# Performance work log

Measured on AMD Instinct MI355X. Metric: run time of the kernel, lower is better.

## Reference

```python
import jax, jax.numpy as jnp
import numpy as np

B, FEAT = 2048, 256
NUM_PIDS, CQ_SIZE = 30000, 8192
MOMENTUM = 0.5
SCALAR = 30.0
EPS_BN = 1e-5      # BatchNorm1d default eps
EPS_NORM = 1e-12   # F.normalize default eps


def l2norm(x):
    n = jnp.linalg.norm(x, axis=1, keepdims=True)
    return x / jnp.maximum(n, EPS_NORM)


def setup_inputs() -> dict:
    key = jax.random.key(0)
    k1, k2, k3, k4 = jax.random.split(key, 4)
    inputs = jax.random.normal(k1, (B, FEAT), jnp.float32)
    label = jax.random.randint(k2, (B,), 0, NUM_PIDS + 1)  # NUM_PIDS == ignore_index
    lut = jax.random.normal(k3, (NUM_PIDS, FEAT), jnp.float32)
    cq = jax.random.normal(k4, (CQ_SIZE, FEAT), jnp.float32)
    bn_weight = jnp.ones((FEAT,), jnp.float32)
    bn_bias = jnp.zeros((FEAT,), jnp.float32)
    return {"inputs": inputs, "label": label, "lut": lut, "cq": cq,
            "bn_weight": bn_weight, "bn_bias": bn_bias}


def reference(inputs, label, lut, cq, bn_weight, bn_bias):
    dtype = inputs.dtype
    rows = jnp.arange(B)

    # --- eval-mode BN on inputs (running stats at init: mean=0, var=1) ---
    norm_inputs = inputs / jnp.sqrt(jnp.asarray(1.0 + EPS_BN, dtype)) * bn_weight + bn_bias

    # --- bad-row masks (rows that are all zero) ---
    bad_lut_mask = jnp.all(lut == 0, axis=1)            # [P]
    good_lut = ~bad_lut_mask
    lc = jnp.minimum(label, NUM_PIDS - 1)
    bad_pos_mask = (label < NUM_PIDS) & bad_lut_mask[lc]  # label hits a bad lut row

    # --- train-mode masked BN over good lut rows (momentum=1.0 => running stats = batch stats) ---
    gm = good_lut[:, None].astype(dtype)
    n = jnp.sum(gm)
    mean = jnp.sum(lut * gm, axis=0) / n
    var = jnp.sum(((lut - mean) ** 2) * gm, axis=0) / n  # biased var for normalization
    lut_bn = jnp.where(good_lut[:, None],
                       (lut - mean) / jnp.sqrt(var + EPS_BN) * bn_weight + bn_bias,
                       lut)
    # running stats update happens under the hood (detached); unbiased var
    rm1 = jax.lax.stop_gradient(mean)
    rv1 = jax.lax.stop_gradient(var * n / (n - 1.0))

    qn = l2norm(norm_inputs)                              # [B, F]
    out_lab = qn @ l2norm(lut_bn).T                       # [B, P]
    out_lab = jnp.where(bad_lut_mask[None, :], jnp.asarray(-1.0, dtype), out_lab)
    out_lab = out_lab.at[rows, lc].set(
        jnp.where(bad_pos_mask, jnp.asarray(1.0, dtype), out_lab[rows, lc]))

    # --- eval-mode masked BN on cq using the just-updated running stats ---
    bad_cq_mask = jnp.all(cq == 0, axis=1)                # [Q]
    cq_bn = jnp.where(~bad_cq_mask[:, None],
                      (cq - rm1) / jnp.sqrt(rv1 + EPS_BN) * bn_weight + bn_bias,
                      cq)
    out_unl = qn @ l2norm(cq_bn).T                        # [B, Q]
    out_unl = jnp.where(bad_cq_mask[None, :], jnp.asarray(-1.0, dtype), out_unl)

    projected = jnp.concatenate([out_lab, out_unl], axis=1) * jnp.asarray(SCALAR, dtype)

    # --- cross entropy with ignore_index = NUM_PIDS, reduction='none', then sum/B ---
    logp = jax.nn.log_softmax(projected, axis=1)
    valid = label != NUM_PIDS
    per = -logp[rows, jnp.where(valid, label, 0)]
    per = jnp.where(valid, per, jnp.asarray(0.0, dtype))
    loss = jnp.sum(per) / B

    # --- serial momentum scatter into lut + circular-buffer enqueue into cq ---
    xs = jax.lax.stop_gradient(inputs)
    lut0 = jax.lax.stop_gradient(lut)
    cq0 = jax.lax.stop_gradient(cq)

    def step(carry, xy):
        lut_c, cq_c, hdr = carry
        x, y = xy
        is_lab = y < NUM_PIDS
        yc = jnp.minimum(y, NUM_PIDS - 1)
        new_row = jnp.where(is_lab, MOMENTUM * lut_c[yc] + (1.0 - MOMENTUM) * x, lut_c[yc])
        lut_c = lut_c.at[yc].set(new_row)
        cq_row = jnp.where(is_lab, cq_c[hdr], x)
        cq_c = cq_c.at[hdr].set(cq_row)
        hdr = jnp.where(is_lab, hdr, (hdr + 1) % CQ_SIZE)
        return (lut_c, cq_c, hdr), None

    (new_lut, new_cq, _), _ = jax.lax.scan(
        step, (lut0, cq0, jnp.asarray(0, label.dtype)), (xs, label))

    return loss, new_lut, new_cq
```

## Files before the change

kernel.cpp:

```cpp
#include <hip/hip_runtime.h>
#include <math.h>

#define NUM_PIDS 30000
#define CQ_SIZE  8192
#define BATCH    2048
#define FEAT     256
#define EPS_BN   1e-5f
#define EPS_NORM 1e-12f
#define SCALARV  30.0f

#define LUT_PAD  30080
#define NCOL     38272
#define BC       128
#define LUT_TILES 235
#define CT       299
#define RT       16
#define NWG      (CT*RT)
#define NB1      240
#define ROWS1    125
#define QPLANE   (BATCH*FEAT)

#define WS_Q1    0
#define WS_CB1   (WS_Q1 + BATCH*FEAT)
#define WS_CB2   (WS_CB1 + BATCH)
#define WS_RN2   (WS_CB2 + BATCH)
#define WS_FLAGS (WS_RN2 + 2*NCOL)
#define WS_PSUM  (WS_FLAGS + LUT_PAD)
#define WS_PSQ   (WS_PSUM + NB1*FEAT)
#define WS_PCNT  (WS_PSQ + NB1*FEAT)
#define WS_A1    (WS_PCNT + 256)
#define WS_B1    (WS_A1 + FEAT)
#define WS_A2    (WS_B1 + FEAT)
#define WS_B2    (WS_A2 + FEAT)
#define WS_ZT    (WS_B2 + FEAT)
#define WS_PART  (WS_ZT + BATCH)
#define WS_LOSS8 (WS_PART + BATCH*CT)
#define WS_XH    ((WS_LOSS8 + 8 + 3) & ~3)
#define WS_XL    (WS_XH + NCOL*FEAT/2)
#define WS_QP    (WS_XL + NCOL*FEAT/2)

typedef __bf16 bf16x8 __attribute__((ext_vector_type(8)));
typedef float  f32x4  __attribute__((ext_vector_type(4)));

__device__ __forceinline__ unsigned short f2bf(float f) {
  __bf16 h = (__bf16)f; return __builtin_bit_cast(unsigned short, h);
}
__device__ __forceinline__ float bf2f(unsigned short u) {
  __bf16 h = __builtin_bit_cast(__bf16, u); return (float)h;
}
__device__ __forceinline__ void gload_lds16(const void* g, void* l) {
  __builtin_amdgcn_global_load_lds((__attribute__((address_space(1))) void*)(g),
                                   (__attribute__((address_space(3))) void*)(l), 16, 0, 0);
}

__global__ __launch_bounds__(256) void k_stats1(const float* __restrict__ lut,
                                                float* __restrict__ ws,
                                                int* __restrict__ flags) {
  const int t = threadIdx.x;
  const int rbase = blockIdx.x * ROWS1;
  __shared__ unsigned char wz[ROWS1 * 4];
  float s = 0.f, sq = 0.f;
  for (int i = 0; i < ROWS1; ++i) {
    float v = lut[(size_t)(rbase + i) * FEAT + t];
    s += v; sq += v * v;
    unsigned long long bal = __ballot(v != 0.0f);
    if ((t & 63) == 0) wz[i * 4 + (t >> 6)] = (bal != 0ull) ? 1 : 0;
  }
  __syncthreads();
  for (int i = t; i < ROWS1; i += 256) {
    int bad = !(wz[i*4] | wz[i*4+1] | wz[i*4+2] | wz[i*4+3]);
    flags[rbase + i] = bad;
  }
  ws[WS_PSUM + blockIdx.x * FEAT + t] = s;
  ws[WS_PSQ  + blockIdx.x * FEAT + t] = sq;
  if (t == 0) {
    int cnt = 0;
    for (int i = 0; i < ROWS1; ++i)
      cnt += (wz[i*4] | wz[i*4+1] | wz[i*4+2] | wz[i*4+3]) ? 1 : 0;
    ws[WS_PCNT + blockIdx.x] = (float)cnt;
  }
}

__global__ __launch_bounds__(256) void k_stats2(const float* __restrict__ bnw,
                                                const float* __restrict__ bnb,
                                                float* __restrict__ ws) {
  const int t = threadIdx.x;
  float2* rn2 = (float2*)(ws + WS_RN2);
  float s = 0.f, sq = 0.f, n = 0.f;
  for (int b = 0; b < NB1; ++b) { s += ws[WS_PSUM + b*FEAT + t]; sq += ws[WS_PSQ + b*FEAT + t]; }
  for (int b = 0; b < NB1; ++b) n += ws[WS_PCNT + b];
  float mean = s / n;
  float var = fmaxf(sq / n - mean * mean, 0.f);
  float istd_b = rsqrtf(var + EPS_BN);
  float rv1 = var * n / (n - 1.f);
  float istd_u = rsqrtf(rv1 + EPS_BN);
  float w = bnw[t], b_ = bnb[t];
  float a1 = istd_b * w, a2 = istd_u * w;
  ws[WS_A1 + t] = a1; ws[WS_B1 + t] = b_ - mean * a1;
  ws[WS_A2 + t] = a2; ws[WS_B2 + t] = b_ - mean * a2;
  if (t < (LUT_PAD - NUM_PIDS)) rn2[NUM_PIDS + t] = make_float2(0.f, -1e30f);
}

__global__ __launch_bounds__(256) void k_prep(const float* __restrict__ lut,
                                              const float* __restrict__ cq,
                                              float* __restrict__ ws,
                                              unsigned short* __restrict__ xh,
                                              unsigned short* __restrict__ xl) {
  const int row = blockIdx.x * 4 + (threadIdx.x >> 6);
  const int ln = threadIdx.x & 63;
  float2* rn2 = (float2*)(ws + WS_RN2);
  if (row >= NUM_PIDS && row < LUT_PAD) {
    uint2 z = make_uint2(0u, 0u);
    *(uint2*)(xh + (size_t)row * FEAT + ln * 4) = z;
    *(uint2*)(xl + (size_t)row * FEAT + ln * 4) = z;
    return;
  }
  const float* src; const float* av; const float* bv;
  if (row < NUM_PIDS) {
    src = lut + (size_t)row * FEAT; av = ws + WS_A1; bv = ws + WS_B1;
  } else {
    src = cq + (size_t)(row - LUT_PAD) * FEAT; av = ws + WS_A2; bv = ws + WS_B2;
  }
  float4 x = ((const float4*)src)[ln];
  float4 a = ((const float4*)av)[ln];
  float4 b = ((const float4*)bv)[ln];
  unsigned short h0 = f2bf(x.x), h1 = f2bf(x.y), h2 = f2bf(x.z), h3 = f2bf(x.w);
  unsigned short l0 = f2bf(x.x - bf2f(h0)), l1 = f2bf(x.y - bf2f(h1));
  unsigned short l2 = f2bf(x.z - bf2f(h2)), l3 = f2bf(x.w - bf2f(h3));
  *(uint2*)(xh + (size_t)row * FEAT + ln * 4) =
      make_uint2((unsigned)h0 | ((unsigned)h1 << 16), (unsigned)h2 | ((unsigned)h3 << 16));
  *(uint2*)(xl + (size_t)row * FEAT + ln * 4) =
      make_uint2((unsigned)l0 | ((unsigned)l1 << 16), (unsigned)l2 | ((unsigned)l3 << 16));
  bool nz = (x.x != 0.f) || (x.y != 0.f) || (x.z != 0.f) || (x.w != 0.f);
  unsigned long long bal = __ballot(nz);
  float t0 = a.x*x.x + b.x, t1 = a.y*x.y + b.y, t2 = a.z*x.z + b.z, t3 = a.w*x.w + b.w;
  float ssum = t0*t0 + t1*t1 + t2*t2 + t3*t3;
  for (int o = 32; o; o >>= 1) ssum += __shfl_xor(ssum, o);
  if (ln == 0) {
    rn2[row] = (bal == 0ull) ? make_float2(0.f, -SCALARV)
                             : make_float2(1.0f / fmaxf(sqrtf(ssum), EPS_NORM), 1e30f);
  }
}

__global__ __launch_bounds__(256) void k_qn(const float* __restrict__ inp,
                                            const float* __restrict__ bnw,
                                            const float* __restrict__ bnb,
                                            float* __restrict__ ws,
                                            unsigned short* __restrict__ qp) {
  const int r = blockIdx.x, t = threadIdx.x;
  const float s0 = rsqrtf(1.0f + EPS_BN);
  float v = inp[(size_t)r * FEAT + t];
  float bn = v * (bnw[t] * s0) + bnb[t];
  float x = bn * bn;
  for (int o = 32; o; o >>= 1) x += __shfl_down(x, o);
  __shared__ float w4[4];
  __shared__ float w8[8];
  if ((t & 63) == 0) w4[t >> 6] = x;
  __syncthreads();
  float nsq = w4[0] + w4[1] + w4[2] + w4[3];
  float rinv = 1.0f / fmaxf(sqrtf(nsq), EPS_NORM);
  float qn = bn * rinv;
  float y1 = qn * ws[WS_B1 + t], y2 = qn * ws[WS_B2 + t];
  for (int o = 32; o; o >>= 1) { y1 += __shfl_down(y1, o); y2 += __shfl_down(y2, o); }
  if ((t & 63) == 0) { w8[t >> 6] = y1; w8[4 + (t >> 6)] = y2; }
  float q1 = qn * ws[WS_A1 + t], q2 = qn * ws[WS_A2 + t];
  ws[WS_Q1 + (size_t)r * FEAT + t] = q1;
  size_t o1 = (size_t)r * FEAT + t;
  unsigned short h1 = f2bf(q1), h2 = f2bf(q2);
  qp[0*QPLANE + o1] = h1;
  qp[1*QPLANE + o1] = f2bf(q1 - bf2f(h1));
  qp[2*QPLANE + o1] = h2;
  qp[3*QPLANE + o1] = f2bf(q2 - bf2f(h2));
  __syncthreads();
  if (t == 0) {
    ws[WS_CB1 + r] = w8[0] + w8[1] + w8[2] + w8[3];
    ws[WS_CB2 + r] = w8[4] + w8[5] + w8[6] + w8[7];
  }
}

__global__ __launch_bounds__(256, 3) void k_gemm(const unsigned short* __restrict__ xh,
                                                 const unsigned short* __restrict__ xl,
                                                 const unsigned short* __restrict__ qp,
                                                 float* __restrict__ ws) {
  __shared__ __align__(16) unsigned char smem[32768];
  const int tid = threadIdx.x;
  const int w = tid >> 6, l = tid & 63;
  const int bid = blockIdx.x;
  const int sid = (bid & 7) * (NWG / 8) + (bid >> 3);
  const int colT = sid >> 4, rowT = sid & 15;
  const bool islut = colT < LUT_TILES;
  const int colbase = colT * BC;
  const int rowbase = rowT * 128;

  const unsigned short* qh = qp + (islut ? 0 : 2) * QPLANE;
  const unsigned short* ql = qh + QPLANE;

  const unsigned short* sg = (w & 1) ? xl : xh;
  unsigned char* sl = smem + (w & 1) * 16384 + (w >> 1) * 8192;
  const int segc = l >> 3;
  const int kc8l = (l & 7) ^ segc;
  const unsigned short* gp =
      sg + (size_t)(colbase + (w >> 1) * 64 + segc) * FEAT + kc8l * 8;

  const int lc = l & 15, lk = l >> 4;
  const int wr = w >> 1, wc = w & 1;
  const size_t qbase = (size_t)(rowbase + wr * 64 + lc) * FEAT;

  f32x4 acc[4][4];
#pragma unroll
  for (int rf = 0; rf < 4; ++rf)
#pragma unroll
    for (int cf = 0; cf < 4; ++cf) { f32x4 z = {0.f,0.f,0.f,0.f}; acc[rf][cf] = z; }

  for (int kc = 0; kc < 4; ++kc) {
    const int kb = kc * 64;
#pragma unroll
    for (int i = 0; i < 8; ++i)
      gload_lds16(gp + (size_t)i * 8 * FEAT + kb, sl + i * 1024);
    __syncthreads();
#pragma unroll
    for (int ks = 0; ks < 2; ++ks) {
      const int kc8 = ks * 4 + lk;
      const int sA = (kc8 ^ (lc & 7)) * 16;
      bf16x8 ah[4], al[4], bh[4], bl[4];
#pragma unroll
      for (int rf = 0; rf < 4; ++rf) {
        size_t qa = qbase + rf * 16 * FEAT + kb + kc8 * 8;
        ah[rf] = *(const bf16x8*)(qh + qa);
        al[rf] = *(const bf16x8*)(ql + qa);
      }
#pragma unroll
      for (int cf = 0; cf < 4; ++cf) {
        int off = (wc * 64 + cf * 16 + lc) * 128 + sA;
        bh[cf] = *(const bf16x8*)(smem + off);
        bl[cf] = *(const bf16x8*)(smem + 16384 + off);
      }
#pragma unroll
      for (int rf = 0; rf < 4; ++rf)
#pragma unroll
        for (int cf = 0; cf < 4; ++cf) {
          acc[rf][cf] = __builtin_amdgcn_mfma_f32_16x16x32_bf16(ah[rf], bh[cf], acc[rf][cf], 0, 0, 0);
          acc[rf][cf] = __builtin_amdgcn_mfma_f32_16x16x32_bf16(ah[rf], bl[cf], acc[rf][cf], 0, 0, 0);
          acc[rf][cf] = __builtin_amdgcn_mfma_f32_16x16x32_bf16(al[rf], bh[cf], acc[rf][cf], 0, 0, 0);
        }
    }
    __syncthreads();
  }

  const float* cb = ws + (islut ? WS_CB1 : WS_CB2);
  const float2* rn2 = (const float2*)(ws + WS_RN2);
  float* red = (float*)smem;
#pragma unroll
  for (int rf = 0; rf < 4; ++rf) {
    float cbv[4];
#pragma unroll
    for (int r4 = 0; r4 < 4; ++r4)
      cbv[r4] = cb[rowbase + wr * 64 + rf * 16 + lk * 4 + r4];
    float part[4] = {0.f, 0.f, 0.f, 0.f};
#pragma unroll
    for (int cf = 0; cf < 4; ++cf) {
      float2 rc = rn2[colbase + wc * 64 + cf * 16 + lc];
#pragma unroll
      for (int r4 = 0; r4 < 4; ++r4) {
        float z = SCALARV * rc.x * (acc[rf][cf][r4] + cbv[r4]);
        z = fminf(z, rc.y);
        part[r4] += __expf(z - SCALARV);
      }
    }
#pragma unroll
    for (int r4 = 0; r4 < 4; ++r4) {
#pragma unroll
      for (int o = 1; o < 16; o <<= 1) part[r4] += __shfl_xor(part[r4], o);
      if (lc == 0) red[(wr * 64 + rf * 16 + lk * 4 + r4) * 2 + wc] = part[r4];
    }
  }
  __syncthreads();
  if (tid < 128) {
    float val = red[tid * 2] + red[tid * 2 + 1];
    ws[WS_PART + (size_t)colT * BATCH + rowbase + tid] = val;
  }
}

__global__ __launch_bounds__(256) void k_target(const int* __restrict__ label,
                                                const float* __restrict__ lut,
                                                float* __restrict__ ws) {
  const int r = blockIdx.x, t = threadIdx.x;
  const int* flags = (const int*)(ws + WS_FLAGS);
  const float2* rn2 = (const float2*)(ws + WS_RN2);
  int y = label[r];
  if (y >= NUM_PIDS) { if (t == 0) ws[WS_ZT + r] = 0.f; return; }
  if (flags[y] == 1) { if (t == 0) ws[WS_ZT + r] = SCALARV; return; }
  float x = ws[WS_Q1 + (size_t)r * FEAT + t] * lut[(size_t)y * FEAT + t];
  for (int o = 32; o; o >>= 1) x += __shfl_down(x, o);
  __shared__ float w4[4];
  if ((t & 63) == 0) w4[t >> 6] = x;
  __syncthreads();
  if (t == 0) {
    float dot = w4[0] + w4[1] + w4[2] + w4[3];
    ws[WS_ZT + r] = SCALARV * rn2[y].x * (dot + ws[WS_CB1 + r]);
  }
}

__global__ __launch_bounds__(256) void k_loss(const int* __restrict__ label,
                                              float* __restrict__ ws) {
  const int t = threadIdx.x;
  const int r = blockIdx.x * 256 + t;
  const int* flags = (const int*)(ws + WS_FLAGS);
  float ls = 0.f;
  int y = label[r];
  if (y < NUM_PIDS) {
    float ss = 0.f;
    const float* p = ws + WS_PART;
    for (int c = 0; c < CT; ++c) ss += p[(size_t)c * BATCH + r];
    if (flags[y] == 1) ss += 1.0f - __expf(-2.0f * SCALARV);
    ls = (SCALARV + __logf(ss)) - ws[WS_ZT + r];
  }
  for (int o = 32; o; o >>= 1) ls += __shfl_down(ls, o);
  __shared__ float w4[4];
  if ((t & 63) == 0) w4[t >> 6] = ls;
  __syncthreads();
  if (t == 0) ws[WS_LOSS8 + blockIdx.x] = w4[0] + w4[1] + w4[2] + w4[3];
}

__global__ void k_loss2(float* __restrict__ ws, float* __restrict__ out) {
  if (threadIdx.x == 0) {
    float s = 0.f;
    for (int i = 0; i < 8; ++i) s += ws[WS_LOSS8 + i];
    out[0] = s / (float)BATCH;
  }
}

__global__ __launch_bounds__(256) void k_lutupd(const int* __restrict__ label,
                                                const float* __restrict__ inp,
                                                const float* __restrict__ lut,
                                                float* __restrict__ out_lut) {
  const int r = blockIdx.x, t = threadIdx.x;
  const int y = label[r];
  if (y >= NUM_PIDS) return;
  __shared__ unsigned long long mask[32];
  const int wv = t >> 6, ln = t & 63;
#pragma unroll
  for (int it = 0; it < 8; ++it) {
    int i = it * 256 + wv * 64 + ln;
    unsigned long long bal = __ballot(label[i] == y);
    if (ln == 0) mask[it * 4 + wv] = bal;
  }
  __syncthreads();
  const int wr_ = r >> 6, br_ = r & 63;
  unsigned long long selfbit = 1ull << br_;
  bool after = (mask[wr_] & ~((selfbit - 1) | selfbit)) != 0ull;
  for (int w2 = wr_ + 1; w2 < 32; ++w2) after = after || (mask[w2] != 0ull);
  if (after) return;
  float f = lut[(size_t)y * FEAT + t];
  for (int w2 = 0; w2 <= wr_; ++w2) {
    unsigned long long m = mask[w2];
    if (w2 == wr_) m &= (selfbit - 1) | selfbit;
    while (m) {
      int b = __ffsll((unsigned long long)m) - 1;
      m &= m - 1;
      int rr = w2 * 64 + b;
      f = 0.5f * f + 0.5f * inp[(size_t)rr * FEAT + t];
    }
  }
  out_lut[(size_t)y * FEAT + t] = f;
}

__global__ __launch_bounds__(256) void k_cqupd(const int* __restrict__ label,
                                               const float* __restrict__ inp,
                                               float* __restrict__ out_cq) {
  const int r = blockIdx.x, t = threadIdx.x;
  if (label[r] != NUM_PIDS) return;
  __shared__ unsigned long long mask[32];
  const int wv = t >> 6, ln = t & 63;
#pragma unroll
  for (int it = 0; it < 8; ++it) {
    int i = it * 256 + wv * 64 + ln;
    unsigned long long bal = __ballot(label[i] == NUM_PIDS);
    if (ln == 0) mask[it * 4 + wv] = bal;
  }
  __syncthreads();
  const int wr_ = r >> 6, br_ = r & 63;
  int rank = 0;
  for (int w2 = 0; w2 < wr_; ++w2) rank += __popcll(mask[w2]);
  rank += __popcll(mask[wr_] & ((1ull << br_) - 1ull));
  out_cq[(size_t)rank * FEAT + t] = inp[(size_t)r * FEAT + t];
}

extern "C" void kernel_launch(void* const* d_in, const int* in_sizes, int n_in,
                              void* d_out, int out_size, void* d_ws, size_t ws_size,
                              hipStream_t stream) {
  const float* inp = (const float*)d_in[0];
  const int* label = (const int*)d_in[1];
  const float* lut = (const float*)d_in[2];
  const float* cq  = (const float*)d_in[3];
  const float* bnw = (const float*)d_in[4];
  const float* bnb = (const float*)d_in[5];
  float* out = (float*)d_out;
  float* ws  = (float*)d_ws;
  int* flags = (int*)(ws + WS_FLAGS);
  unsigned short* xh = (unsigned short*)(ws + WS_XH);
  unsigned short* xl = (unsigned short*)(ws + WS_XL);
  unsigned short* qp = (unsigned short*)(ws + WS_QP);

  float* out_lut = out + 1;
  float* out_cq  = out + 1 + (size_t)NUM_PIDS * FEAT;

  hipMemcpyAsync(out_lut, lut, (size_t)NUM_PIDS * FEAT * sizeof(float),
                 hipMemcpyDeviceToDevice, stream);
  hipMemcpyAsync(out_cq, cq, (size_t)CQ_SIZE * FEAT * sizeof(float),
                 hipMemcpyDeviceToDevice, stream);

  k_stats1<<<NB1, 256, 0, stream>>>(lut, ws, flags);
  k_stats2<<<1, 256, 0, stream>>>(bnw, bnb, ws);
  k_prep<<<NCOL / 4, 256, 0, stream>>>(lut, cq, ws, xh, xl);
  k_qn<<<BATCH, 256, 0, stream>>>(inp, bnw, bnb, ws, qp);
  k_gemm<<<NWG, 256, 0, stream>>>(xh, xl, qp, ws);
  k_target<<<BATCH, 256, 0, stream>>>(label, lut, ws);
  k_loss<<<8, 256, 0, stream>>>(label, ws);
  k_loss2<<<1, 64, 0, stream>>>(ws, out);
  k_lutupd<<<BATCH, 256, 0, stream>>>(label, inp, lut, out_lut);
  k_cqupd<<<BATCH, 256, 0, stream>>>(label, inp, out_cq);
}
```

Baseline: 383.3 us.

## Fuse output copies into prep, target into qn, stage Q tiles in LDS

The separate device-to-device copies of lut and cq into the outputs are removed and done inside k_prep, which already reads every row. The target-logit dot product moves into k_qn, which drops the fp32 Q workspace write, and the lut and cq update kernels are merged into one launched before the GEMM. The GEMM now stages both Q planes into a 64KB LDS buffer instead of reading them from global memory per fragment, and drops its occupancy hint of 3. The changes cut launches and redundant memory traffic, at the cost of larger LDS use that may lower GEMM occupancy.

Measured after the change: 347.4 us. 9.4% less time.

```diff
diff --git a/kernel.cpp b/kernel.cpp
--- a/kernel.cpp
+++ b/kernel.cpp
@@ -105,7 +105,9 @@
                                               const float* __restrict__ cq,
                                               float* __restrict__ ws,
                                               unsigned short* __restrict__ xh,
-                                              unsigned short* __restrict__ xl) {
+                                              unsigned short* __restrict__ xl,
+                                              float* __restrict__ out_lut,
+                                              float* __restrict__ out_cq) {
   const int row = blockIdx.x * 4 + (threadIdx.x >> 6);
   const int ln = threadIdx.x & 63;
   float2* rn2 = (float2*)(ws + WS_RN2);
@@ -115,15 +117,18 @@
     *(uint2*)(xl + (size_t)row * FEAT + ln * 4) = z;
     return;
   }
-  const float* src; const float* av; const float* bv;
+  const float* src; const float* av; const float* bv; float* dst;
   if (row < NUM_PIDS) {
     src = lut + (size_t)row * FEAT; av = ws + WS_A1; bv = ws + WS_B1;
+    dst = out_lut + (size_t)row * FEAT;
   } else {
     src = cq + (size_t)(row - LUT_PAD) * FEAT; av = ws + WS_A2; bv = ws + WS_B2;
+    dst = out_cq + (size_t)(row - LUT_PAD) * FEAT;
   }
   float4 x = ((const float4*)src)[ln];
   float4 a = ((const float4*)av)[ln];
   float4 b = ((const float4*)bv)[ln];
+  dst[ln*4+0] = x.x; dst[ln*4+1] = x.y; dst[ln*4+2] = x.z; dst[ln*4+3] = x.w;
   unsigned short h0 = f2bf(x.x), h1 = f2bf(x.y), h2 = f2bf(x.z), h3 = f2bf(x.w);
   unsigned short l0 = f2bf(x.x - bf2f(h0)), l1 = f2bf(x.y - bf2f(h1));
   unsigned short l2 = f2bf(x.z - bf2f(h2)), l3 = f2bf(x.w - bf2f(h3));
@@ -145,6 +150,8 @@
 __global__ __launch_bounds__(256) void k_qn(const float* __restrict__ inp,
                                             const float* __restrict__ bnw,
                                             const float* __restrict__ bnb,
+                                            const int* __restrict__ label,
+                                            const float* __restrict__ lut,
                                             float* __restrict__ ws,
                                             unsigned short* __restrict__ qp) {
   const int r = blockIdx.x, t = threadIdx.x;
@@ -155,6 +162,7 @@
   for (int o = 32; o; o >>= 1) x += __shfl_down(x, o);
   __shared__ float w4[4];
   __shared__ float w8[8];
+  __shared__ float w4b[4];
   if ((t & 63) == 0) w4[t >> 6] = x;
   __syncthreads();
   float nsq = w4[0] + w4[1] + w4[2] + w4[3];
@@ -164,7 +172,6 @@
   for (int o = 32; o; o >>= 1) { y1 += __shfl_down(y1, o); y2 += __shfl_down(y2, o); }
   if ((t & 63) == 0) { w8[t >> 6] = y1; w8[4 + (t >> 6)] = y2; }
   float q1 = qn * ws[WS_A1 + t], q2 = qn * ws[WS_A2 + t];
-  ws[WS_Q1 + (size_t)r * FEAT + t] = q1;
   size_t o1 = (size_t)r * FEAT + t;
   unsigned short h1 = f2bf(q1), h2 = f2bf(q2);
   qp[0*QPLANE + o1] = h1;
@@ -176,13 +183,27 @@
     ws[WS_CB1 + r] = w8[0] + w8[1] + w8[2] + w8[3];
     ws[WS_CB2 + r] = w8[4] + w8[5] + w8[6] + w8[7];
   }
-}
-
-__global__ __launch_bounds__(256, 3) void k_gemm(const unsigned short* __restrict__ xh,
-                                                 const unsigned short* __restrict__ xl,
-                                                 const unsigned short* __restrict__ qp,
-                                                 float* __restrict__ ws) {
-  __shared__ __align__(16) unsigned char smem[32768];
+  const int* flags = (const int*)(ws + WS_FLAGS);
+  const float2* rn2 = (const float2*)(ws + WS_RN2);
+  int y = label[r];
+  if (y >= NUM_PIDS) { if (t == 0) ws[WS_ZT + r] = 0.f; return; }
+  if (flags[y] == 1) { if (t == 0) ws[WS_ZT + r] = SCALARV; return; }
+  float xt = q1 * lut[(size_t)y * FEAT + t];
+  for (int o = 32; o; o >>= 1) xt += __shfl_down(xt, o);
+  if ((t & 63) == 0) w4b[t >> 6] = xt;
+  __syncthreads();
+  if (t == 0) {
+    float dot = w4b[0] + w4b[1] + w4b[2] + w4b[3];
+    float cb1 = w8[0] + w8[1] + w8[2] + w8[3];
+    ws[WS_ZT + r] = SCALARV * rn2[y].x * (dot + cb1);
+  }
+}
+
+__global__ __launch_bounds__(256) void k_gemm(const unsigned short* __restrict__ xh,
+                                              const unsigned short* __restrict__ xl,
+                                              const unsigned short* __restrict__ qp,
+                                              float* __restrict__ ws) {
+  __shared__ __align__(16) unsigned char smem[65536];
   const int tid = threadIdx.x;
   const int w = tid >> 6, l = tid & 63;
   const int bid = blockIdx.x;
@@ -195,16 +216,18 @@
   const unsigned short* qh = qp + (islut ? 0 : 2) * QPLANE;
   const unsigned short* ql = qh + QPLANE;
 
-  const unsigned short* sg = (w & 1) ? xl : xh;
-  unsigned char* sl = smem + (w & 1) * 16384 + (w >> 1) * 8192;
-  const int segc = l >> 3;
-  const int kc8l = (l & 7) ^ segc;
-  const unsigned short* gp =
-      sg + (size_t)(colbase + (w >> 1) * 64 + segc) * FEAT + kc8l * 8;
+  const int segc = l >> 3, slot = l & 7;
+  const int kc8l = slot ^ segc;
+  const unsigned short* gsrc;
+  unsigned char* lbase;
+  int gbase;
+  if (w == 0)      { gsrc = xh; lbase = smem;         gbase = colbase; }
+  else if (w == 1) { gsrc = xl; lbase = smem + 16384; gbase = colbase; }
+  else if (w == 2) { gsrc = qh; lbase = smem + 32768; gbase = rowbase; }
+  else             { gsrc = ql; lbase = smem + 49152; gbase = rowbase; }
 
   const int lc = l & 15, lk = l >> 4;
   const int wr = w >> 1, wc = w & 1;
-  const size_t qbase = (size_t)(rowbase + wr * 64 + lc) * FEAT;
 
   f32x4 acc[4][4];
 #pragma unroll
@@ -215,8 +238,10 @@
   for (int kc = 0; kc < 4; ++kc) {
     const int kb = kc * 64;
 #pragma unroll
-    for (int i = 0; i < 8; ++i)
-      gload_lds16(gp + (size_t)i * 8 * FEAT + kb, sl + i * 1024);
+    for (int i = 0; i < 16; ++i) {
+      const unsigned short* g = gsrc + (size_t)(gbase + i * 8 + segc) * FEAT + kb + kc8l * 8;
+      gload_lds16(g, lbase + i * 1024);
+    }
     __syncthreads();
 #pragma unroll
     for (int ks = 0; ks < 2; ++ks) {
@@ -225,9 +250,9 @@
       bf16x8 ah[4], al[4], bh[4], bl[4];
 #pragma unroll
       for (int rf = 0; rf < 4; ++rf) {
-        size_t qa = qbase + rf * 16 * FEAT + kb + kc8 * 8;
-        ah[rf] = *(const bf16x8*)(qh + qa);
-        al[rf] = *(const bf16x8*)(ql + qa);
+        int off = (wr * 64 + rf * 16 + lc) * 128 + sA;
+        ah[rf] = *(const bf16x8*)(smem + 32768 + off);
+        al[rf] = *(const bf16x8*)(smem + 49152 + off);
       }
 #pragma unroll
       for (int cf = 0; cf < 4; ++cf) {
@@ -278,26 +303,6 @@
   if (tid < 128) {
     float val = red[tid * 2] + red[tid * 2 + 1];
     ws[WS_PART + (size_t)colT * BATCH + rowbase + tid] = val;
-  }
-}
-
-__global__ __launch_bounds__(256) void k_target(const int* __restrict__ label,
-                                                const float* __restrict__ lut,
-                                                float* __restrict__ ws) {
-  const int r = blockIdx.x, t = threadIdx.x;
-  const int* flags = (const int*)(ws + WS_FLAGS);
-  const float2* rn2 = (const float2*)(ws + WS_RN2);
-  int y = label[r];
-  if (y >= NUM_PIDS) { if (t == 0) ws[WS_ZT + r] = 0.f; return; }
-  if (flags[y] == 1) { if (t == 0) ws[WS_ZT + r] = SCALARV; return; }
-  float x = ws[WS_Q1 + (size_t)r * FEAT + t] * lut[(size_t)y * FEAT + t];
-  for (int o = 32; o; o >>= 1) x += __shfl_down(x, o);
-  __shared__ float w4[4];
-  if ((t & 63) == 0) w4[t >> 6] = x;
-  __syncthreads();
-  if (t == 0) {
-    float dot = w4[0] + w4[1] + w4[2] + w4[3];
-    ws[WS_ZT + r] = SCALARV * rn2[y].x * (dot + ws[WS_CB1 + r]);
   }
 }
 
@@ -330,60 +335,53 @@
   }
 }
 
-__global__ __launch_bounds__(256) void k_lutupd(const int* __restrict__ label,
-                                                const float* __restrict__ inp,
-                                                const float* __restrict__ lut,
-                                                float* __restrict__ out_lut) {
+__global__ __launch_bounds__(256) void k_lutcq(const int* __restrict__ label,
+                                               const float* __restrict__ inp,
+                                               const float* __restrict__ lut,
+                                               float* __restrict__ out_lut,
+                                               float* __restrict__ out_cq) {
   const int r = blockIdx.x, t = threadIdx.x;
   const int y = label[r];
-  if (y >= NUM_PIDS) return;
   __shared__ unsigned long long mask[32];
   const int wv = t >> 6, ln = t & 63;
-#pragma unroll
-  for (int it = 0; it < 8; ++it) {
-    int i = it * 256 + wv * 64 + ln;
-    unsigned long long bal = __ballot(label[i] == y);
-    if (ln == 0) mask[it * 4 + wv] = bal;
-  }
-  __syncthreads();
   const int wr_ = r >> 6, br_ = r & 63;
-  unsigned long long selfbit = 1ull << br_;
-  bool after = (mask[wr_] & ~((selfbit - 1) | selfbit)) != 0ull;
-  for (int w2 = wr_ + 1; w2 < 32; ++w2) after = after || (mask[w2] != 0ull);
-  if (after) return;
-  float f = lut[(size_t)y * FEAT + t];
-  for (int w2 = 0; w2 <= wr_; ++w2) {
-    unsigned long long m = mask[w2];
-    if (w2 == wr_) m &= (selfbit - 1) | selfbit;
-    while (m) {
-      int b = __ffsll((unsigned long long)m) - 1;
-      m &= m - 1;
-      int rr = w2 * 64 + b;
-      f = 0.5f * f + 0.5f * inp[(size_t)rr * FEAT + t];
-    }
-  }
-  out_lut[(size_t)y * FEAT + t] = f;
-}
-
-__global__ __launch_bounds__(256) void k_cqupd(const int* __restrict__ label,
-                                               const float* __restrict__ inp,
-                                               float* __restrict__ out_cq) {
-  const int r = blockIdx.x, t = threadIdx.x;
-  if (label[r] != NUM_PIDS) return;
-  __shared__ unsigned long long mask[32];
-  const int wv = t >> 6, ln = t & 63;
-#pragma unroll
-  for (int it = 0; it < 8; ++it) {
-    int i = it * 256 + wv * 64 + ln;
-    unsigned long long bal = __ballot(label[i] == NUM_PIDS);
-    if (ln == 0) mask[it * 4 + wv] = bal;
-  }
-  __syncthreads();
-  const int wr_ = r >> 6, br_ = r & 63;
-  int rank = 0;
-  for (int w2 = 0; w2 < wr_; ++w2) rank += __popcll(mask[w2]);
-  rank += __popcll(mask[wr_] & ((1ull << br_) - 1ull));
-  out_cq[(size_t)rank * FEAT + t] = inp[(size_t)r * FEAT + t];
+  if (y < NUM_PIDS) {
+#pragma unroll
+    for (int it = 0; it < 8; ++it) {
+      int i = it * 256 + wv * 64 + ln;
+      unsigned long long bal = __ballot(label[i] == y);
+      if (ln == 0) mask[it * 4 + wv] = bal;
+    }
+    __syncthreads();
+    unsigned long long selfbit = 1ull << br_;
+    bool after = (mask[wr_] & ~((selfbit - 1) | selfbit)) != 0ull;
+    for (int w2 = wr_ + 1; w2 < 32; ++w2) after = after || (mask[w2] != 0ull);
+    if (after) return;
+    float f = lut[(size_t)y * FEAT + t];
+    for (int w2 = 0; w2 <= wr_; ++w2) {
+      unsigned long long m = mask[w2];
+      if (w2 == wr_) m &= (selfbit - 1) | selfbit;
+      while (m) {
+        int b = __ffsll((unsigned long long)m) - 1;
+        m &= m - 1;
+        int rr = w2 * 64 + b;
+        f = 0.5f * f + 0.5f * inp[(size_t)rr * FEAT + t];
+      }
+    }
+    out_lut[(size_t)y * FEAT + t] = f;
+  } else {
+#pragma unroll
+    for (int it = 0; it < 8; ++it) {
+      int i = it * 256 + wv * 64 + ln;
+      unsigned long long bal = __ballot(label[i] == NUM_PIDS);
+      if (ln == 0) mask[it * 4 + wv] = bal;
+    }
+    __syncthreads();
+    int rank = 0;
+    for (int w2 = 0; w2 < wr_; ++w2) rank += __popcll(mask[w2]);
+    rank += __popcll(mask[wr_] & ((1ull << br_) - 1ull));
+    out_cq[(size_t)rank * FEAT + t] = inp[(size_t)r * FEAT + t];
+  }
 }
 
 extern "C" void kernel_launch(void* const* d_in, const int* in_sizes, int n_in,
@@ -405,19 +403,12 @@
   float* out_lut = out + 1;
   float* out_cq  = out + 1 + (size_t)NUM_PIDS * FEAT;
 
-  hipMemcpyAsync(out_lut, lut, (size_t)NUM_PIDS * FEAT * sizeof(float),
-                 hipMemcpyDeviceToDevice, stream);
-  hipMemcpyAsync(out_cq, cq, (size_t)CQ_SIZE * FEAT * sizeof(float),
-                 hipMemcpyDeviceToDevice, stream);
-
   k_stats1<<<NB1, 256, 0, stream>>>(lut, ws, flags);
   k_stats2<<<1, 256, 0, stream>>>(bnw, bnb, ws);
-  k_prep<<<NCOL / 4, 256, 0, stream>>>(lut, cq, ws, xh, xl);
-  k_qn<<<BATCH, 256, 0, stream>>>(inp, bnw, bnb, ws, qp);
+  k_prep<<<NCOL / 4, 256, 0, stream>>>(lut, cq, ws, xh, xl, out_lut, out_cq);
+  k_qn<<<BATCH, 256, 0, stream>>>(inp, bnw, bnb, label, lut, ws, qp);
+  k_lutcq<<<BATCH, 256, 0, stream>>>(label, inp, lut, out_lut, out_cq);
   k_gemm<<<NWG, 256, 0, stream>>>(xh, xl, qp, ws);
-  k_target<<<BATCH, 256, 0, stream>>>(label, lut, ws);
   k_loss<<<8, 256, 0, stream>>>(label, ws);
   k_loss2<<<1, 64, 0, stream>>>(ws, out);
-  k_lutupd<<<BATCH, 256, 0, stream>>>(label, inp, lut, out_lut);
-  k_cqupd<<<BATCH, 256, 0, stream>>>(label, inp, out_cq);
-}
+}
```
